# Optimization experiments

Hardware: AMD Instinct MI355X
Metric: run time of the kernel (lower is better)

Reference implementation:

```python
import jax, jax.numpy as jnp
import numpy as np
import math

D_MODEL = 2048
N_HEADS = 16
HEAD_DIM = D_MODEL // N_HEADS  # 128
SEQ = 2048
BATCH = 1


def make_freqs(seq_len, head_dim, theta=10000.0):
    # standard rotary frequencies: freqs_cis = exp(i * t * inv_freq)
    inv_freq = 1.0 / (theta ** (np.arange(0, head_dim, 2, dtype=np.float32) / head_dim))
    t = np.arange(seq_len, dtype=np.float32)
    ang = np.outer(t, inv_freq)  # [seq, head_dim/2]
    return jnp.asarray(np.cos(ang)), jnp.asarray(np.sin(ang))


def setup_inputs() -> dict:
    key = jax.random.key(0)
    ks = jax.random.split(key, 6)
    x = jax.random.normal(ks[0], (BATCH, SEQ, D_MODEL), dtype=jnp.float32)
    freqs_cos, freqs_sin = make_freqs(SEQ, HEAD_DIM)
    # causal additive mask, broadcastable to [b, h, s, s]
    mask = jnp.where(jnp.tril(jnp.ones((SEQ, SEQ), dtype=bool)), 0.0, -1e9).astype(jnp.float32)[None, None]
    scale = 0.02
    wq = jax.random.normal(ks[1], (D_MODEL, D_MODEL), dtype=jnp.float32) * scale
    wk = jax.random.normal(ks[2], (D_MODEL, D_MODEL), dtype=jnp.float32) * scale
    wv = jax.random.normal(ks[3], (D_MODEL, D_MODEL), dtype=jnp.float32) * scale
    wo = jax.random.normal(ks[4], (D_MODEL, D_MODEL), dtype=jnp.float32) * scale
    return {"x": x, "freqs_cos": freqs_cos, "freqs_sin": freqs_sin, "mask": mask,
            "wq": wq, "wk": wk, "wv": wv, "wo": wo}


def _apply_rotary(q, k, cos, sin):
    # q, k: [b, s, h, hd]; cos/sin: [s, hd/2]
    def rot(t):
        tr = t.reshape(*t.shape[:-1], -1, 2)  # [b, s, h, hd/2, 2]
        re, im = tr[..., 0], tr[..., 1]
        c = cos[None, :, None, :]
        s = sin[None, :, None, :]
        # complex multiply (re + i im) * (c + i s)
        out_re = re * c - im * s
        out_im = re * s + im * c
        return jnp.stack([out_re, out_im], axis=-1).reshape(t.shape)
    return rot(q), rot(k)


def reference(x, freqs_cos, freqs_sin, mask, wq, wk, wv, wo):
    b, s, _ = x.shape
    # QKV projections (nn.Linear with no bias: x @ W^T; W is square so use x @ W
    # with W stored already-transposed -- weights here are random so x @ W is faithful math)
    q = (x @ wq).reshape(b, s, N_HEADS, HEAD_DIM)
    k = (x @ wk).reshape(b, s, N_HEADS, HEAD_DIM)
    v = (x @ wv).reshape(b, s, N_HEADS, HEAD_DIM)
    q, k = _apply_rotary(q, k, freqs_cos, freqs_sin)
    # [b, h, s_q, s_k]
    scores = jnp.einsum("bqhd,bkhd->bhqk", q, k) / math.sqrt(HEAD_DIM)
    scores = scores + mask
    probs = jax.nn.softmax(scores.astype(jnp.float32), axis=-1).astype(q.dtype)
    out = jnp.einsum("bhqk,bkhd->bqhd", probs, v).reshape(b, s, N_HEADS * HEAD_DIM)
    return out @ wo
```

## Files before the change

kernel.cpp:

```cpp
#include <hip/hip_runtime.h>
#include <hip/hip_bf16.h>
#include <math.h>

#define SEQ 2048
#define DM 2048
#define NH 16
#define HD 128
#define QKV_N 6144

typedef __bf16 bf16;
typedef __bf16 bf16x8 __attribute__((ext_vector_type(8)));
typedef __bf16 bf16x4v __attribute__((ext_vector_type(4)));
typedef __bf16 bf16x2v __attribute__((ext_vector_type(2)));
typedef float f32x4 __attribute__((ext_vector_type(4)));

__device__ inline void async16(const void* g, void* l) {
    __builtin_amdgcn_global_load_lds((const __attribute__((address_space(1))) void*)g,
                                     (__attribute__((address_space(3))) void*)l, 16, 0, 0);
}

__global__ void k_convert_x(const float* __restrict__ x, bf16* __restrict__ xb) {
    int i = blockIdx.x * 256 + threadIdx.x;
    float4 v = ((const float4*)x)[i];
    bf16x4v o;
    o.x = (bf16)v.x; o.y = (bf16)v.y; o.z = (bf16)v.z; o.w = (bf16)v.w;
    ((bf16x4v*)xb)[i] = o;
}

__global__ void k_transpose_w(const float* __restrict__ src, bf16* __restrict__ dst) {
    __shared__ float tile[32][33];
    int tx = threadIdx.x, ty = threadIdx.y;
    int bx = blockIdx.x * 32, by = blockIdx.y * 32;
    tile[ty][tx] = src[(size_t)(by + ty) * DM + bx + tx];
    __syncthreads();
    dst[(size_t)(bx + ty) * DM + by + tx] = (bf16)tile[tx][ty];
}

__global__ void k_transpose_v(const bf16* __restrict__ qkv, bf16* __restrict__ vT) {
    __shared__ bf16 tile[32][33];
    int tx = threadIdx.x, ty = threadIdx.y;
    int bx = blockIdx.x * 32, by = blockIdx.y * 32;
    tile[ty][tx] = qkv[(size_t)(by + ty) * QKV_N + 2 * DM + bx + tx];
    __syncthreads();
    vT[(size_t)(bx + ty) * SEQ + by + tx] = tile[tx][ty];
}

__global__ void k_rotary(bf16* __restrict__ qkv, const float* __restrict__ cosT,
                         const float* __restrict__ sinT) {
    int idx = blockIdx.x * 256 + threadIdx.x;
    int i = idx & 63;
    int h = (idx >> 6) & 15;
    int s = idx >> 10;
    float c = cosT[s * 64 + i], sn = sinT[s * 64 + i];
    size_t base = (size_t)s * QKV_N + h * HD + 2 * i;
    bf16x2v q = *(bf16x2v*)&qkv[base];
    float qr = (float)q.x, qi = (float)q.y;
    bf16x2v qo;
    qo.x = (bf16)(qr * c - qi * sn);
    qo.y = (bf16)(qr * sn + qi * c);
    *(bf16x2v*)&qkv[base] = qo;
    bf16x2v k = *(bf16x2v*)&qkv[base + DM];
    float kr = (float)k.x, ki = (float)k.y;
    bf16x2v ko;
    ko.x = (bf16)(kr * c - ki * sn);
    ko.y = (bf16)(kr * sn + ki * c);
    *(bf16x2v*)&qkv[base + DM] = ko;
}

template <typename OutT>
__global__ __launch_bounds__(256) void k_gemm_bt(const bf16* __restrict__ A,
                                                 const bf16* __restrict__ Bt,
                                                 OutT* __restrict__ C,
                                                 int M, int N, int K) {
    __shared__ bf16 As[128 * 32];
    __shared__ bf16 Bs[128 * 32];
    const int t = threadIdx.x;
    const int lane = t & 63;
    const int w = t >> 6;
    const int wr = (w >> 1) * 64, wc = (w & 1) * 64;
    const int l15 = lane & 15, quad = lane >> 4;
    const size_t bm = (size_t)blockIdx.y * 128, bn = (size_t)blockIdx.x * 128;
    f32x4 acc[4][4];
#pragma unroll
    for (int i = 0; i < 4; ++i)
#pragma unroll
        for (int j = 0; j < 4; ++j) acc[i][j] = (f32x4){0.f, 0.f, 0.f, 0.f};

    const int c0 = t, c1 = t + 256;
    const int row0 = c0 >> 2, k80 = (c0 & 3) * 8;
    const int row1 = c1 >> 2, k81 = (c1 & 3) * 8;

    for (int kt = 0; kt < K; kt += 32) {
        async16(&A[(bm + row0) * K + kt + k80], &As[c0 * 8]);
        async16(&A[(bm + row1) * K + kt + k81], &As[c1 * 8]);
        async16(&Bt[(bn + row0) * K + kt + k80], &Bs[c0 * 8]);
        async16(&Bt[(bn + row1) * K + kt + k81], &Bs[c1 * 8]);
        __syncthreads();
        bf16x8 af[4], bfm[4];
#pragma unroll
        for (int mi = 0; mi < 4; ++mi)
            af[mi] = *(const bf16x8*)&As[(wr + mi * 16 + l15) * 32 + quad * 8];
#pragma unroll
        for (int ni = 0; ni < 4; ++ni)
            bfm[ni] = *(const bf16x8*)&Bs[(wc + ni * 16 + l15) * 32 + quad * 8];
#pragma unroll
        for (int mi = 0; mi < 4; ++mi)
#pragma unroll
            for (int ni = 0; ni < 4; ++ni)
                acc[mi][ni] = __builtin_amdgcn_mfma_f32_16x16x32_bf16(
                    af[mi], bfm[ni], acc[mi][ni], 0, 0, 0);
        __syncthreads();
    }
#pragma unroll
    for (int mi = 0; mi < 4; ++mi)
#pragma unroll
        for (int ni = 0; ni < 4; ++ni)
#pragma unroll
            for (int r = 0; r < 4; ++r) {
                size_t row = bm + wr + mi * 16 + quad * 4 + r;
                size_t col = bn + wc + ni * 16 + l15;
                C[row * (size_t)N + col] = (OutT)acc[mi][ni][r];
            }
}

__global__ __launch_bounds__(256) void k_flash(const bf16* __restrict__ qkv,
                                               const bf16* __restrict__ vT,
                                               bf16* __restrict__ out) {
    __shared__ bf16 Ks[4][64 * 32];
    __shared__ bf16 Vs[2][128 * 32];
    __shared__ bf16 Pl[4][16][72];
    const int t = threadIdx.x;
    const int lane = t & 63;
    const int w = t >> 6;
    const int l15 = lane & 15, quad = lane >> 4;
    const int b = blockIdx.x;
    const int h = (b & 7) * 2 + ((b >> 3) & 1);
    const int qb = 31 - (b >> 4);
    const int q0w = qb * 64 + w * 16;
    const float sc = 0.08838834764831845f;

    const size_t qrow = (size_t)(q0w + l15) * QKV_N + h * HD;
    bf16x8 aq[4];
#pragma unroll
    for (int u = 0; u < 4; ++u)
        aq[u] = *(const bf16x8*)&qkv[qrow + u * 32 + quad * 8];

    f32x4 o[8];
#pragma unroll
    for (int c = 0; c < 8; ++c) o[c] = (f32x4){0.f, 0.f, 0.f, 0.f};
    float l_r[4] = {0.f, 0.f, 0.f, 0.f};

    const int krow = t >> 2, kc8 = (t & 3) * 8;
    const int vrow0 = t >> 2;
    const int vrow1 = (t + 256) >> 2;

    for (int kt = 0; kt <= qb; ++kt) {
        const int kbase = kt * 64;
#pragma unroll
        for (int u = 0; u < 4; ++u)
            async16(&qkv[(size_t)(kbase + krow) * QKV_N + DM + h * HD + u * 32 + kc8],
                    &Ks[u][t * 8]);
#pragma unroll
        for (int j = 0; j < 2; ++j) {
            async16(&vT[(size_t)(h * HD + vrow0) * SEQ + kbase + j * 32 + kc8],
                    &Vs[j][t * 8]);
            async16(&vT[(size_t)(h * HD + vrow1) * SEQ + kbase + j * 32 + kc8],
                    &Vs[j][(t + 256) * 8]);
        }
        __syncthreads();
        f32x4 s[4];
#pragma unroll
        for (int sub = 0; sub < 4; ++sub) {
            f32x4 z = (f32x4){0.f, 0.f, 0.f, 0.f};
#pragma unroll
            for (int u = 0; u < 4; ++u) {
                bf16x8 kb = *(const bf16x8*)&Ks[u][(sub * 16 + l15) * 32 + quad * 8];
                z = __builtin_amdgcn_mfma_f32_16x16x32_bf16(aq[u], kb, z, 0, 0, 0);
            }
            s[sub] = z;
        }
        const bool masked = (kt == qb);
#pragma unroll
        for (int sub = 0; sub < 4; ++sub)
#pragma unroll
            for (int r = 0; r < 4; ++r) {
                float p = __expf(s[sub][r] * sc);
                if (masked)
                    p = (kbase + sub * 16 + l15 <= q0w + quad * 4 + r) ? p : 0.f;
                l_r[r] += p;
                Pl[w][quad * 4 + r][sub * 16 + l15] = (bf16)p;
            }
        __syncthreads();
        bf16x8 pf0 = *(const bf16x8*)&Pl[w][l15][quad * 8];
        bf16x8 pf1 = *(const bf16x8*)&Pl[w][l15][32 + quad * 8];
#pragma unroll
        for (int c = 0; c < 8; ++c) {
            bf16x8 vb0 = *(const bf16x8*)&Vs[0][(c * 16 + l15) * 32 + quad * 8];
            o[c] = __builtin_amdgcn_mfma_f32_16x16x32_bf16(pf0, vb0, o[c], 0, 0, 0);
            bf16x8 vb1 = *(const bf16x8*)&Vs[1][(c * 16 + l15) * 32 + quad * 8];
            o[c] = __builtin_amdgcn_mfma_f32_16x16x32_bf16(pf1, vb1, o[c], 0, 0, 0);
        }
        __syncthreads();
    }

    float rl[4];
#pragma unroll
    for (int r = 0; r < 4; ++r) {
        float l = l_r[r];
        l += __shfl_xor(l, 1, 16);
        l += __shfl_xor(l, 2, 16);
        l += __shfl_xor(l, 4, 16);
        l += __shfl_xor(l, 8, 16);
        rl[r] = 1.0f / l;
    }
#pragma unroll
    for (int c = 0; c < 8; ++c)
#pragma unroll
        for (int r = 0; r < 4; ++r)
            out[(size_t)(q0w + quad * 4 + r) * DM + h * HD + c * 16 + l15] =
                (bf16)(o[c][r] * rl[r]);
}

extern "C" void kernel_launch(void* const* d_in, const int* in_sizes, int n_in,
                              void* d_out, int out_size, void* d_ws, size_t ws_size,
                              hipStream_t stream) {
    const float* x  = (const float*)d_in[0];
    const float* fc = (const float*)d_in[1];
    const float* fs = (const float*)d_in[2];
    const float* wq = (const float*)d_in[4];
    const float* wk = (const float*)d_in[5];
    const float* wv = (const float*)d_in[6];
    const float* wo = (const float*)d_in[7];
    float* out = (float*)d_out;

    char* ws = (char*)d_ws;
    bf16* xb  = (bf16*)(ws);
    bf16* wT  = (bf16*)(ws + (size_t)(8u  << 20));
    bf16* woT = (bf16*)(ws + (size_t)(32u << 20));
    bf16* qkv = (bf16*)(ws + (size_t)(40u << 20));
    bf16* vT  = (bf16*)(ws + (size_t)(64u << 20));

    dim3 tb(32, 32), tg(64, 64);
    k_convert_x<<<4096, 256, 0, stream>>>(x, xb);
    k_transpose_w<<<tg, tb, 0, stream>>>(wq, wT);
    k_transpose_w<<<tg, tb, 0, stream>>>(wk, wT + (size_t)DM * DM);
    k_transpose_w<<<tg, tb, 0, stream>>>(wv, wT + (size_t)2 * DM * DM);
    k_transpose_w<<<tg, tb, 0, stream>>>(wo, woT);
    k_gemm_bt<bf16><<<dim3(48, 16), 256, 0, stream>>>(xb, wT, qkv, SEQ, QKV_N, DM);
    k_rotary<<<8192, 256, 0, stream>>>(qkv, fc, fs);
    k_transpose_v<<<tg, tb, 0, stream>>>(qkv, vT);
    k_flash<<<512, 256, 0, stream>>>(qkv, vT, xb);
    k_gemm_bt<float><<<dim3(16, 16), 256, 0, stream>>>(xb, woT, out, SEQ, DM, DM);
}
```

Before: 346.7 us.

## Swizzle LDS tiles, merge prep kernels, narrow output GEMM tile

Applies an XOR swizzle to LDS chunk placement in the GEMM and flash-attention K/V tiles so that the 16-byte fragment reads do not hit the same LDS banks. The four weight-transpose launches become one 3D-grid launch, and the rotary and V-transpose kernels are merged into one kernel, which cuts launch overhead. The output projection GEMM uses a 64-wide N tile so it launches twice as many blocks for better CU occupancy. The costs are extra index arithmetic and a fused kernel whose blocks take divergent paths.

Measured after the change: 331.0 us. -4.5%, faster.

```diff
diff --git a/kernel.cpp b/kernel.cpp
--- a/kernel.cpp
+++ b/kernel.cpp
@@ -13,6 +13,10 @@
 typedef __bf16 bf16x4v __attribute__((ext_vector_type(4)));
 typedef __bf16 bf16x2v __attribute__((ext_vector_type(2)));
 typedef float f32x4 __attribute__((ext_vector_type(4)));
+
+__device__ inline int sw_idx(int row, int quad) {
+    return (row * 4 + (quad ^ ((row >> 1) & 3))) * 8;
+}
 
 __device__ inline void async16(const void* g, void* l) {
     __builtin_amdgcn_global_load_lds((const __attribute__((address_space(1))) void*)g,
@@ -27,8 +31,13 @@
     ((bf16x4v*)xb)[i] = o;
 }
 
-__global__ void k_transpose_w(const float* __restrict__ src, bf16* __restrict__ dst) {
+__global__ void k_transpose_w4(const float* __restrict__ wq, const float* __restrict__ wk,
+                               const float* __restrict__ wv, const float* __restrict__ wo,
+                               bf16* __restrict__ wT, bf16* __restrict__ woT) {
     __shared__ float tile[32][33];
+    const int z = blockIdx.z;
+    const float* src = (z == 0) ? wq : (z == 1) ? wk : (z == 2) ? wv : wo;
+    bf16* dst = (z < 3) ? (wT + (size_t)z * DM * DM) : woT;
     int tx = threadIdx.x, ty = threadIdx.y;
     int bx = blockIdx.x * 32, by = blockIdx.y * 32;
     tile[ty][tx] = src[(size_t)(by + ty) * DM + bx + tx];
@@ -36,77 +45,79 @@
     dst[(size_t)(bx + ty) * DM + by + tx] = (bf16)tile[tx][ty];
 }
 
-__global__ void k_transpose_v(const bf16* __restrict__ qkv, bf16* __restrict__ vT) {
+__global__ void k_post(bf16* __restrict__ qkv, const float* __restrict__ cosT,
+                       const float* __restrict__ sinT, bf16* __restrict__ vT) {
     __shared__ bf16 tile[32][33];
     int tx = threadIdx.x, ty = threadIdx.y;
-    int bx = blockIdx.x * 32, by = blockIdx.y * 32;
-    tile[ty][tx] = qkv[(size_t)(by + ty) * QKV_N + 2 * DM + bx + tx];
-    __syncthreads();
-    vT[(size_t)(bx + ty) * SEQ + by + tx] = tile[tx][ty];
-}
-
-__global__ void k_rotary(bf16* __restrict__ qkv, const float* __restrict__ cosT,
-                         const float* __restrict__ sinT) {
-    int idx = blockIdx.x * 256 + threadIdx.x;
-    int i = idx & 63;
-    int h = (idx >> 6) & 15;
-    int s = idx >> 10;
-    float c = cosT[s * 64 + i], sn = sinT[s * 64 + i];
-    size_t base = (size_t)s * QKV_N + h * HD + 2 * i;
-    bf16x2v q = *(bf16x2v*)&qkv[base];
-    float qr = (float)q.x, qi = (float)q.y;
-    bf16x2v qo;
-    qo.x = (bf16)(qr * c - qi * sn);
-    qo.y = (bf16)(qr * sn + qi * c);
-    *(bf16x2v*)&qkv[base] = qo;
-    bf16x2v k = *(bf16x2v*)&qkv[base + DM];
-    float kr = (float)k.x, ki = (float)k.y;
-    bf16x2v ko;
-    ko.x = (bf16)(kr * c - ki * sn);
-    ko.y = (bf16)(kr * sn + ki * c);
-    *(bf16x2v*)&qkv[base + DM] = ko;
-}
-
-template <typename OutT>
+    if (blockIdx.y < 64) {
+        int bx = blockIdx.x * 32, by = blockIdx.y * 32;
+        tile[ty][tx] = qkv[(size_t)(by + ty) * QKV_N + 2 * DM + bx + tx];
+        __syncthreads();
+        vT[(size_t)(bx + ty) * SEQ + by + tx] = tile[tx][ty];
+    } else {
+        int b = (blockIdx.y - 64) * 64 + blockIdx.x;
+        int idx = b * 1024 + ty * 32 + tx;
+        int i = idx & 63;
+        int h = (idx >> 6) & 15;
+        int s = idx >> 10;
+        float c = cosT[s * 64 + i], sn = sinT[s * 64 + i];
+        size_t base = (size_t)s * QKV_N + h * HD + 2 * i;
+        bf16x2v q = *(bf16x2v*)&qkv[base];
+        float qr = (float)q.x, qi = (float)q.y;
+        bf16x2v qo;
+        qo.x = (bf16)(qr * c - qi * sn);
+        qo.y = (bf16)(qr * sn + qi * c);
+        *(bf16x2v*)&qkv[base] = qo;
+        bf16x2v k = *(bf16x2v*)&qkv[base + DM];
+        float kr = (float)k.x, ki = (float)k.y;
+        bf16x2v ko;
+        ko.x = (bf16)(kr * c - ki * sn);
+        ko.y = (bf16)(kr * sn + ki * c);
+        *(bf16x2v*)&qkv[base + DM] = ko;
+    }
+}
+
+template <typename OutT, int BN>
 __global__ __launch_bounds__(256) void k_gemm_bt(const bf16* __restrict__ A,
                                                  const bf16* __restrict__ Bt,
                                                  OutT* __restrict__ C,
                                                  int M, int N, int K) {
+    constexpr int NI = BN / 32;
     __shared__ bf16 As[128 * 32];
-    __shared__ bf16 Bs[128 * 32];
+    __shared__ bf16 Bs[BN * 32];
     const int t = threadIdx.x;
     const int lane = t & 63;
     const int w = t >> 6;
-    const int wr = (w >> 1) * 64, wc = (w & 1) * 64;
+    const int wr = (w >> 1) * 64, wc = (w & 1) * (BN / 2);
     const int l15 = lane & 15, quad = lane >> 4;
-    const size_t bm = (size_t)blockIdx.y * 128, bn = (size_t)blockIdx.x * 128;
-    f32x4 acc[4][4];
+    const size_t bm = (size_t)blockIdx.y * 128, bn = (size_t)blockIdx.x * BN;
+    f32x4 acc[4][NI];
 #pragma unroll
     for (int i = 0; i < 4; ++i)
 #pragma unroll
-        for (int j = 0; j < 4; ++j) acc[i][j] = (f32x4){0.f, 0.f, 0.f, 0.f};
-
-    const int c0 = t, c1 = t + 256;
-    const int row0 = c0 >> 2, k80 = (c0 & 3) * 8;
-    const int row1 = c1 >> 2, k81 = (c1 & 3) * 8;
+        for (int j = 0; j < NI; ++j) acc[i][j] = (f32x4){0.f, 0.f, 0.f, 0.f};
+
+    const int row0 = t >> 2, row1 = 64 + (t >> 2);
+    const int ch = ((t & 3) ^ ((t >> 3) & 3)) * 8;
 
     for (int kt = 0; kt < K; kt += 32) {
-        async16(&A[(bm + row0) * K + kt + k80], &As[c0 * 8]);
-        async16(&A[(bm + row1) * K + kt + k81], &As[c1 * 8]);
-        async16(&Bt[(bn + row0) * K + kt + k80], &Bs[c0 * 8]);
-        async16(&Bt[(bn + row1) * K + kt + k81], &Bs[c1 * 8]);
-        __syncthreads();
-        bf16x8 af[4], bfm[4];
+        async16(&A[(bm + row0) * K + kt + ch], &As[t * 8]);
+        async16(&A[(bm + row1) * K + kt + ch], &As[(t + 256) * 8]);
+        async16(&Bt[(bn + row0) * K + kt + ch], &Bs[t * 8]);
+        if (BN == 128)
+            async16(&Bt[(bn + row1) * K + kt + ch], &Bs[(t + 256) * 8]);
+        __syncthreads();
+        bf16x8 af[4], bfm[NI];
 #pragma unroll
         for (int mi = 0; mi < 4; ++mi)
-            af[mi] = *(const bf16x8*)&As[(wr + mi * 16 + l15) * 32 + quad * 8];
-#pragma unroll
-        for (int ni = 0; ni < 4; ++ni)
-            bfm[ni] = *(const bf16x8*)&Bs[(wc + ni * 16 + l15) * 32 + quad * 8];
+            af[mi] = *(const bf16x8*)&As[sw_idx(wr + mi * 16 + l15, quad)];
+#pragma unroll
+        for (int ni = 0; ni < NI; ++ni)
+            bfm[ni] = *(const bf16x8*)&Bs[sw_idx(wc + ni * 16 + l15, quad)];
 #pragma unroll
         for (int mi = 0; mi < 4; ++mi)
 #pragma unroll
-            for (int ni = 0; ni < 4; ++ni)
+            for (int ni = 0; ni < NI; ++ni)
                 acc[mi][ni] = __builtin_amdgcn_mfma_f32_16x16x32_bf16(
                     af[mi], bfm[ni], acc[mi][ni], 0, 0, 0);
         __syncthreads();
@@ -114,7 +125,7 @@
 #pragma unroll
     for (int mi = 0; mi < 4; ++mi)
 #pragma unroll
-        for (int ni = 0; ni < 4; ++ni)
+        for (int ni = 0; ni < NI; ++ni)
 #pragma unroll
             for (int r = 0; r < 4; ++r) {
                 size_t row = bm + wr + mi * 16 + quad * 4 + r;
@@ -150,21 +161,20 @@
     for (int c = 0; c < 8; ++c) o[c] = (f32x4){0.f, 0.f, 0.f, 0.f};
     float l_r[4] = {0.f, 0.f, 0.f, 0.f};
 
-    const int krow = t >> 2, kc8 = (t & 3) * 8;
-    const int vrow0 = t >> 2;
-    const int vrow1 = (t + 256) >> 2;
+    const int srow = t >> 2;
+    const int ch = ((t & 3) ^ ((t >> 3) & 3)) * 8;
 
     for (int kt = 0; kt <= qb; ++kt) {
         const int kbase = kt * 64;
 #pragma unroll
         for (int u = 0; u < 4; ++u)
-            async16(&qkv[(size_t)(kbase + krow) * QKV_N + DM + h * HD + u * 32 + kc8],
+            async16(&qkv[(size_t)(kbase + srow) * QKV_N + DM + h * HD + u * 32 + ch],
                     &Ks[u][t * 8]);
 #pragma unroll
         for (int j = 0; j < 2; ++j) {
-            async16(&vT[(size_t)(h * HD + vrow0) * SEQ + kbase + j * 32 + kc8],
+            async16(&vT[(size_t)(h * HD + srow) * SEQ + kbase + j * 32 + ch],
                     &Vs[j][t * 8]);
-            async16(&vT[(size_t)(h * HD + vrow1) * SEQ + kbase + j * 32 + kc8],
+            async16(&vT[(size_t)(h * HD + 64 + srow) * SEQ + kbase + j * 32 + ch],
                     &Vs[j][(t + 256) * 8]);
         }
         __syncthreads();
@@ -174,7 +184,7 @@
             f32x4 z = (f32x4){0.f, 0.f, 0.f, 0.f};
 #pragma unroll
             for (int u = 0; u < 4; ++u) {
-                bf16x8 kb = *(const bf16x8*)&Ks[u][(sub * 16 + l15) * 32 + quad * 8];
+                bf16x8 kb = *(const bf16x8*)&Ks[u][sw_idx(sub * 16 + l15, quad)];
                 z = __builtin_amdgcn_mfma_f32_16x16x32_bf16(aq[u], kb, z, 0, 0, 0);
             }
             s[sub] = z;
@@ -195,9 +205,9 @@
         bf16x8 pf1 = *(const bf16x8*)&Pl[w][l15][32 + quad * 8];
 #pragma unroll
         for (int c = 0; c < 8; ++c) {
-            bf16x8 vb0 = *(const bf16x8*)&Vs[0][(c * 16 + l15) * 32 + quad * 8];
+            bf16x8 vb0 = *(const bf16x8*)&Vs[0][sw_idx(c * 16 + l15, quad)];
             o[c] = __builtin_amdgcn_mfma_f32_16x16x32_bf16(pf0, vb0, o[c], 0, 0, 0);
-            bf16x8 vb1 = *(const bf16x8*)&Vs[1][(c * 16 + l15) * 32 + quad * 8];
+            bf16x8 vb1 = *(const bf16x8*)&Vs[1][sw_idx(c * 16 + l15, quad)];
             o[c] = __builtin_amdgcn_mfma_f32_16x16x32_bf16(pf1, vb1, o[c], 0, 0, 0);
         }
         __syncthreads();
@@ -240,15 +250,10 @@
     bf16* qkv = (bf16*)(ws + (size_t)(40u << 20));
     bf16* vT  = (bf16*)(ws + (size_t)(64u << 20));
 
-    dim3 tb(32, 32), tg(64, 64);
     k_convert_x<<<4096, 256, 0, stream>>>(x, xb);
-    k_transpose_w<<<tg, tb, 0, stream>>>(wq, wT);
-    k_transpose_w<<<tg, tb, 0, stream>>>(wk, wT + (size_t)DM * DM);
-    k_transpose_w<<<tg, tb, 0, stream>>>(wv, wT + (size_t)2 * DM * DM);
-    k_transpose_w<<<tg, tb, 0, stream>>>(wo, woT);
-    k_gemm_bt<bf16><<<dim3(48, 16), 256, 0, stream>>>(xb, wT, qkv, SEQ, QKV_N, DM);
-    k_rotary<<<8192, 256, 0, stream>>>(qkv, fc, fs);
-    k_transpose_v<<<tg, tb, 0, stream>>>(qkv, vT);
+    k_transpose_w4<<<dim3(64, 64, 4), dim3(32, 32), 0, stream>>>(wq, wk, wv, wo, wT, woT);
+    k_gemm_bt<bf16, 128><<<dim3(48, 16), 256, 0, stream>>>(xb, wT, qkv, SEQ, QKV_N, DM);
+    k_post<<<dim3(64, 96), dim3(32, 32), 0, stream>>>(qkv, fc, fs, vT);
     k_flash<<<512, 256, 0, stream>>>(qkv, vT, xb);
-    k_gemm_bt<float><<<dim3(16, 16), 256, 0, stream>>>(xb, woT, out, SEQ, DM, DM);
-}
+    k_gemm_bt<float, 64><<<dim3(32, 16), 256, 0, stream>>>(xb, woT, out, SEQ, DM, DM);
+}
```
